# Performance work log

Hardware: AMD Instinct MI355X
Metric: run time of the kernel (lower is better)

Reference implementation:

```python
import jax, jax.numpy as jnp
import numpy as np

N_CLASS, N_SUPPORT, N_QUERY = 64, 5, 64
D_IN, C, WIN = 1024, 128, 5
D = C * WIN * WIN  # 3200, fine-encoder output dim


def setup_inputs() -> dict:
    key = jax.random.key(0)
    ks = jax.random.split(key, 6)
    s = 0.02  # weight init scale
    return {
        "xs": jax.random.normal(ks[0], (N_CLASS, N_SUPPORT, D_IN), jnp.float32),
        "xq": jax.random.normal(ks[1], (N_CLASS, N_QUERY, D_IN), jnp.float32),
        "W_share": jax.random.normal(ks[2], (D_IN, D), jnp.float32) * s,
        "b_share": jnp.zeros((D,), jnp.float32),
        "W_att": jax.random.normal(ks[3], (C, C), jnp.float32) * s,
        "b_att": jnp.zeros((C,), jnp.float32),
        "W_fine": jax.random.normal(ks[4], (D, D), jnp.float32) * s,
        "b_fine": jnp.zeros((D,), jnp.float32),
    }


def reference(xs, xq, W_share, b_share, W_att, b_att, W_fine, b_fine):
    n_class, n_support = xs.shape[0], xs.shape[1]
    n_query = xq.shape[1]
    ns = n_class * n_support

    # concat support + query, run shared encoder
    x = jnp.concatenate([xs.reshape(ns, -1), xq.reshape(n_class * n_query, -1)], axis=0)
    z_share = jax.nn.relu(x @ W_share + b_share)            # [N, D]
    z4 = z_share.reshape(-1, C, WIN, WIN)

    # attention head: spatial mean -> linear -> per-channel logits
    z_att = z4.mean(axis=(2, 3)) @ W_att + b_att            # [N, C]

    diag_c = jax.nn.softmax(z_att[:ns].mean(axis=0)) * C    # [C]
    w = jnp.repeat(diag_c, WIN * WIN)                       # [D] diagonal of learned metric

    # fine encoder (flatten + linear)
    z = z_share @ W_fine + b_fine                           # [N, D]
    z_proto = z[:ns].reshape(n_class, n_support, -1).mean(axis=1)  # [n_class, D]
    zq = z[ns:]                                             # [n, D]

    # attentionMetric with diagonal metric == weighted squared distance:
    # dists[i,j] = sum_d w_d (zq_i - proto_j)^2, expanded to avoid the n*m*d diff tensor
    q2 = (zq * zq) @ w                                      # [n]
    p2 = (z_proto * z_proto) @ w                            # [m]
    cross = (zq * w) @ z_proto.T                            # [n, m]
    dists = q2[:, None] + p2[None, :] - 2.0 * cross         # [n, m]

    log_p_y = jax.nn.log_softmax(-dists, axis=1).reshape(n_class, n_query, n_class)
    target = jnp.arange(n_class)
    tgt = jnp.broadcast_to(target[:, None, None], (n_class, n_query, 1))
    loss_val = -jnp.take_along_axis(log_p_y, tgt, axis=2).mean()
    y_hat = jnp.argmax(log_p_y, axis=2)
    acc_val = (y_hat == target[:, None]).astype(jnp.float32).mean()
    return loss_val, acc_val
```

## Files before the change

### kernel.cpp

```cpp
#include <hip/hip_runtime.h>
#include <math.h>

#define N_CLASS 64
#define N_SUPPORT 5
#define N_QUERY 64
#define D_IN 1024
#define C_CH 128
#define WIN 5
#define D_FEAT 3200
#define NS 320
#define NQ 4096
#define M_ROWS 4416
#define M_PAD 4480

#define ZP_SLICE  (N_CLASS * D_FEAT)
#define GT_SLICE  (128 * D_FEAT)
#define CR_SLICE  (NQ * 128)
#define NKS       10
#define LOSS_BLKS (NQ / 4)

#define PREP_X   4480
#define PREP_WS  800
#define CONV64   2500
#define GEMM8_BLKS (35 * 25)

#define WS_SCALE    64.0f
#define WS_INVSCALE 0.015625f

#define WS_XF8      0u
#define WS_WSF8     4718592u
#define WS_ZSB      8126464u
#define WS_WFB      36388864u
#define WS_WFTB     56868864u
#define WS_ARENA    77348864u
#define WS_UB       98320384u
#define WS_YB       99139584u
#define WS_GT       99958784u
#define WS_WV       100777984u
#define WS_P2       100790784u
#define WS_CVEC     100791296u
#define WS_LPART    100791808u
#define WS_UPOOL    100800128u


typedef __bf16 bf16x8 __attribute__((ext_vector_type(8)));
typedef __bf16 bf16x4 __attribute__((ext_vector_type(4)));
typedef float floatx4 __attribute__((ext_vector_type(4)));
typedef __attribute__((address_space(1))) const void* gptr_t;
typedef __attribute__((address_space(3))) void* lptr_t;

__device__ __forceinline__ float waveReduceSum(float v) {
    for (int off = 32; off > 0; off >>= 1) v += __shfl_xor(v, off, 64);
    return v;
}

__global__ __launch_bounds__(256) void prep_kernel(const float* __restrict__ xs,
                                                   const float* __restrict__ xq,
                                                   const float* __restrict__ W_share,
                                                   unsigned char* __restrict__ Xf8,
                                                   unsigned char* __restrict__ Wsf8)
{
    __shared__ float tile[64][65];
    const int b = blockIdx.x;
    const int t = threadIdx.x;

    if (b < PREP_X) {
        const int e = (b * 256 + t) * 4;
        const int row = e >> 10;
        const int col = e & 1023;
        float4 v = make_float4(0.f, 0.f, 0.f, 0.f);
        if (row < NS)          v = *(const float4*)(xs + (size_t)row * D_IN + col);
        else if (row < M_ROWS) v = *(const float4*)(xq + (size_t)(row - NS) * D_IN + col);
        int p = __builtin_amdgcn_cvt_pk_fp8_f32(v.x, v.y, 0, false);
        p     = __builtin_amdgcn_cvt_pk_fp8_f32(v.z, v.w, p, true);
        const int ocol = col ^ (((row >> 1) & 1) << 3);
        *(int*)(Xf8 + (size_t)row * D_IN + ocol) = p;
        return;
    }
    const int tx = t & 63;
    const int ty = t >> 6;
    const int tb = b - PREP_X;
    const int n0 = (tb % 50) * 64;
    const int k0 = (tb / 50) * 64;
#pragma unroll
    for (int i = ty; i < 64; i += 4)
        tile[i][tx] = W_share[(size_t)(k0 + i) * D_FEAT + n0 + tx];
    __syncthreads();
#pragma unroll
    for (int i = ty; i < 64; i += 4) {
        const int p = __builtin_amdgcn_cvt_pk_fp8_f32(tile[tx][i] * WS_SCALE, 0.f,
                                                      0, false);
        const int n = n0 + i;
        const int k = (k0 + tx) ^ (((n >> 1) & 1) << 3);
        Wsf8[(size_t)n * D_IN + k] = (unsigned char)(p & 0xff);
    }
}

__global__ __launch_bounds__(256, 3) void gemm_fp8_128(const unsigned char* __restrict__ A,
                                                       const unsigned char* __restrict__ Bt,
                                                       const float* __restrict__ bias,
                                                       __bf16* __restrict__ out_bf)
{
    __shared__ __align__(16) unsigned char smem[49152];

    const int t    = threadIdx.x;
    const int lane = t & 63;
    const int w    = t >> 6;
    const int wm   = w >> 1;
    const int wn   = w & 1;

    const int bx = blockIdx.x % 25;
    const int by = blockIdx.x / 25;
    const int bm = by * 128;
    const int bn = bx * 128;

    const int q    = lane >> 4;
    const int r16  = lane & 15;
    const int m3   = (r16 >> 1) & 7;
    const int off0 = (q ^ m3) * 8;

    const int rowA = (wm * 64 + r16) * 64;
    const int rowB = (wn * 64 + r16) * 64;

    const int srow  = t >> 2;
    const int sunit = 16 * ((t & 3) ^ ((srow >> 2) & 3));

    const unsigned char* gA = A  + (size_t)(bm + srow) * D_IN + sunit;
    const unsigned char* gB = Bt + (size_t)(bn + srow) * D_IN + sunit;

    auto stage = [&](int uu, int slot) {
        const unsigned char* ga = gA + uu * 64;
        const unsigned char* gb = gB + uu * 64;
        unsigned char* l = smem + slot * 16384 + t * 16;
        __builtin_amdgcn_global_load_lds((gptr_t)ga,           (lptr_t)l,            16, 0, 0);
        __builtin_amdgcn_global_load_lds((gptr_t)(ga + 65536), (lptr_t)(l + 4096),   16, 0, 0);
        __builtin_amdgcn_global_load_lds((gptr_t)gb,           (lptr_t)(l + 8192),   16, 0, 0);
        __builtin_amdgcn_global_load_lds((gptr_t)(gb + 65536), (lptr_t)(l + 12288),  16, 0, 0);
    };

    floatx4 acc[4][4] = {};
    long av0[4], bv0[4], av1[4], bv1[4];

    auto ld16 = [&](const unsigned char* sa) {
#pragma unroll
        for (int mi = 0; mi < 4; ++mi)
            av0[mi] = *(const long*)(sa + rowA + mi * 1024 + off0);
#pragma unroll
        for (int ni = 0; ni < 4; ++ni)
            bv0[ni] = *(const long*)(sa + 8192 + rowB + ni * 1024 + off0);
#pragma unroll
        for (int mi = 0; mi < 4; ++mi)
            av1[mi] = *(const long*)(sa + rowA + mi * 1024 + (off0 ^ 32));
#pragma unroll
        for (int ni = 0; ni < 4; ++ni)
            bv1[ni] = *(const long*)(sa + 8192 + rowB + ni * 1024 + (off0 ^ 32));
    };
    auto mfma32 = [&]() {
        __builtin_amdgcn_s_setprio(1);
#pragma unroll
        for (int mi = 0; mi < 4; ++mi)
#pragma unroll
            for (int ni = 0; ni < 4; ++ni)
                acc[mi][ni] = __builtin_amdgcn_mfma_f32_16x16x32_fp8_fp8(
                    av0[mi], bv0[ni], acc[mi][ni], 0, 0, 0);
#pragma unroll
        for (int mi = 0; mi < 4; ++mi)
#pragma unroll
            for (int ni = 0; ni < 4; ++ni)
                acc[mi][ni] = __builtin_amdgcn_mfma_f32_16x16x32_fp8_fp8(
                    av1[mi], bv1[ni], acc[mi][ni], 0, 0, 0);
        __builtin_amdgcn_s_setprio(0);
    };

    stage(0, 0);
    stage(1, 1);

    for (int u = 0; u < 14; ++u) {
        const unsigned char* sa = smem + (u % 3) * 16384;
        asm volatile("s_waitcnt vmcnt(4)" ::: "memory");
        __builtin_amdgcn_s_barrier();
        ld16(sa);
        stage(u + 2, (u + 2) % 3);
        asm volatile("s_waitcnt lgkmcnt(0)" ::: "memory");
        mfma32();
    }
    {
        const unsigned char* sa = smem + (14 % 3) * 16384;
        asm volatile("s_waitcnt vmcnt(4)" ::: "memory");
        __builtin_amdgcn_s_barrier();
        ld16(sa);
        asm volatile("s_waitcnt lgkmcnt(0)" ::: "memory");
        mfma32();
    }
    {
        const unsigned char* sa = smem + (15 % 3) * 16384;
        asm volatile("s_waitcnt vmcnt(0)" ::: "memory");
        __builtin_amdgcn_s_barrier();
        ld16(sa);
        asm volatile("s_waitcnt lgkmcnt(0)" ::: "memory");
        mfma32();
    }

    __syncthreads();
    float bcol[4];
#pragma unroll
    for (int ni = 0; ni < 4; ++ni) bcol[ni] = bias[bn + wn * 64 + ni * 16 + r16];
    const int ebase = (wm * 64 + q * 4) * 256 + wn * 128 + r16 * 2;
#pragma unroll
    for (int mi = 0; mi < 4; ++mi)
#pragma unroll
        for (int ni = 0; ni < 4; ++ni) {
            const int cb2 = (ni ^ q) << 5;
#pragma unroll
            for (int reg = 0; reg < 4; ++reg) {
                float v = acc[mi][ni][reg] * WS_INVSCALE + bcol[ni];
                v = fmaxf(v, 0.f);
                *(__bf16*)(smem + ebase + mi * 4096 + reg * 256 + cb2) = (__bf16)v;
            }
        }
    __syncthreads();
#pragma unroll
    for (int ps = 0; ps < 8; ++ps) {
        const int idx  = ps * 256 + t;
        const int row  = idx >> 4;
        const int grow = bm + row;
        if (grow < M_ROWS) {
            const int lb = row * 256 + (((idx & 15) << 4) ^ (((row >> 2) & 3) << 5));
            const int4 d = *(const int4*)(smem + lb);
            *(int4*)((char*)out_bf + ((size_t)grow * D_FEAT + bn + (idx & 15) * 8) * 2) = d;
        }
    }
}

__global__ __launch_bounds__(256) void gemm_bf16(const __bf16* __restrict__ A,
                                                 const __bf16* __restrict__ Bt,
                                                 const float* __restrict__ bias,
                                                 __bf16* __restrict__ out_bf,
                                                 float* __restrict__ out_f32,
                                                 int N, int strideK, int kIters,
                                                 int Mout, int relu, int sliceStride,
                                                 int nbx, int nby, int colLimit,
                                                 const float* __restrict__ attUpool,
                                                 const float* __restrict__ W_att,
                                                 const float* __restrict__ b_att,
                                                 float* __restrict__ wvec)
{
    __shared__ __align__(16) char smem[49152];
    const int t = threadIdx.x;

    if (attUpool != nullptr && blockIdx.x == gridDim.x - 1) {
        float* sW   = (float*)smem;
        float* s_pm = (float*)(smem + 16384);
        float* s_at = (float*)(smem + 16384 + 512);
        float* s_dg = (float*)(smem + 16384 + 1024);
        if (t < C_CH) {
            float a = 0.f;
            for (int p = 0; p < N_CLASS; ++p) a += attUpool[(size_t)p * C_CH + t];
            s_pm[t] = a * (1.0f / (N_CLASS * 25));
        }
        __syncthreads();
        float acc = (t < C_CH) ? b_att[t] : 0.f;
#pragma unroll
        for (int qtr = 0; qtr < 4; ++qtr) {
            const float4* src = (const float4*)(W_att + qtr * 32 * C_CH);
            float4* dst = (float4*)sW;
#pragma unroll
            for (int i = 0; i < 4; ++i) dst[i * 256 + t] = src[i * 256 + t];
            __syncthreads();
            if (t < C_CH) {
#pragma unroll
                for (int k = 0; k < 32; ++k)
                    acc += s_pm[qtr * 32 + k] * sW[k * C_CH + t];
            }
            __syncthreads();
        }
        if (t < C_CH) s_at[t] = acc;
        __syncthreads();
        if (t < C_CH) {
            float m = -INFINITY;
            for (int k = 0; k < C_CH; ++k) m = fmaxf(m, s_at[k]);
            float s = 0.f;
            for (int k = 0; k < C_CH; ++k) s += expf(s_at[k] - m);
            s_dg[t] = expf(acc - m) / s * (float)C_CH;
        }
        __syncthreads();
        for (int j = t; j < D_FEAT; j += 256) wvec[j] = s_dg[j / 25];
        return;
    }

    int bx, by, ks;
    {
        const int nbxy = nbx * nby;
        ks = blockIdx.x / nbxy;
        const int b = blockIdx.x - ks * nbxy;
        const int fg = nbx >> 3;
        const int full = fg * 8 * nby;
        if (b < full) {
            const int g = b / (8 * nby);
            const int r = b - g * 8 * nby;
            bx = g * 8 + (r & 7);
            by = r >> 3;
        } else {
            const int rem = nbx - fg * 8;
            const int r = b - full;
            bx = fg * 8 + r % rem;
            by = r / rem;
        }
    }

    const int lane = t & 63;
    const int w    = t >> 6;
    const int wm   = w >> 1;
    const int wn   = w & 1;
    const int bm   = by * 128;
    const int bn   = bx * 128;

    const int q    = lane >> 4;
    const int r16  = lane & 15;
    const int sw   = (r16 >> 1) & 3;
    const int cA   = (q ^ sw) * 8;

    const int srow   = w * 16 + (lane >> 2);
    const int sglob8 = (((lane & 3) ^ ((lane >> 3) & 3))) * 8;

    const int kBase = ks * kIters * 32;
    floatx4 acc[4][4] = {};

    auto stageb = [&](int ki, int slot) {
        const int k0 = kBase + ki * 32;
        char* base = smem + slot * 16384;
#pragma unroll
        for (int j = 0; j < 2; ++j) {
            const __bf16* ga = A  + (size_t)(bm + j * 64 + srow) * strideK
                                  + k0 + sglob8;
            const __bf16* gb = Bt + (size_t)(bn + j * 64 + srow) * strideK
                                  + k0 + sglob8;
            char* la = base +        j * 4096 + w * 1024;
            char* lb = base + 8192 + j * 4096 + w * 1024;
            __builtin_amdgcn_global_load_lds((gptr_t)ga, (lptr_t)la, 16, 0, 0);
            __builtin_amdgcn_global_load_lds((gptr_t)gb, (lptr_t)lb, 16, 0, 0);
        }
    };

    bf16x8 av[4], bv[4];
    auto ldfrags = [&](const char* base) {
        const __bf16* sAe = (const __bf16*)base;
        const __bf16* sBe = (const __bf16*)(base + 8192);
#pragma unroll
        for (int mi = 0; mi < 4; ++mi)
            av[mi] = *(const bf16x8*)(sAe + ((wm * 64 + mi * 16 + r16) * 32 + cA));
#pragma unroll
        for (int ni = 0; ni < 4; ++ni)
            bv[ni] = *(const bf16x8*)(sBe + ((wn * 64 + ni * 16 + r16) * 32 + cA));
    };
    auto mfma16 = [&]() {
#pragma unroll
        for (int mi = 0; mi < 4; ++mi)
#pragma unroll
            for (int ni = 0; ni < 4; ++ni)
                acc[mi][ni] = __builtin_amdgcn_mfma_f32_16x16x32_bf16(
                    av[mi], bv[ni], acc[mi][ni], 0, 0, 0);
    };

    stageb(0, 0);
    stageb(1, 1);

    for (int u = 0; u < kIters; ++u) {
        const char* base = smem + (u % 3) * 16384;
        if (u + 1 < kIters)
            asm volatile("s_waitcnt vmcnt(4)" ::: "memory");
        else
            asm volatile("s_waitcnt vmcnt(0)" ::: "memory");
        __builtin_amdgcn_s_barrier();
        ldfrags(base);
        if (u + 2 < kIters) stageb(u + 2, (u + 2) % 3);
        asm volatile("s_waitcnt lgkmcnt(0)" ::: "memory");
        mfma16();
    }

#pragma unroll
    for (int ni = 0; ni < 4; ++ni) {
        const int col = bn + wn * 64 + ni * 16 + r16;
        if (col < colLimit) {
            const float bcol = sliceStride ? 0.f : bias[col];
#pragma unroll
            for (int mi = 0; mi < 4; ++mi) {
#pragma unroll
                for (int reg = 0; reg < 4; ++reg) {
                    const int row = bm + wm * 64 + mi * 16 + q * 4 + reg;
                    if (row < Mout) {
                        if (sliceStride) {
                            out_f32[(size_t)ks * sliceStride + (size_t)row * N + col] =
                                acc[mi][ni][reg];
                        } else {
                            float v = acc[mi][ni][reg] + bcol;
                            if (relu) v = fmaxf(v, 0.f);
                            if (out_f32) out_f32[(size_t)row * N + col] = v;
                            else         out_bf [(size_t)row * N + col] = (__bf16)v;
                        }
                    }
                }
            }
        }
    }
}

__global__ __launch_bounds__(256) void ut_conv_kernel(const __bf16* __restrict__ z_share,
                                                      const float* __restrict__ W_fine,
                                                      __bf16* __restrict__ u,
                                                      float* __restrict__ upool,
                                                      __bf16* __restrict__ Wfb,
                                                      __bf16* __restrict__ WfTb)
{
    __shared__ __align__(16) char smem_u[16640];
    const int b = blockIdx.x;
    const int t = threadIdx.x;

    if (b >= 128) {
        float (*tile)[65] = (float(*)[65])smem_u;
        const int tb = b - 128;
        const int tx = t & 63;
        const int ty = t >> 6;
        const int n0 = (tb % 50) * 64;
        const int k0 = (tb / 50) * 64;
#pragma unroll
        for (int i = ty; i < 64; i += 4) {
            const float v = W_fine[(size_t)(k0 + i) * D_FEAT + n0 + tx];
            Wfb[(size_t)(k0 + i) * D_FEAT + n0 + tx] = (__bf16)v;
            tile[i][tx] = v;
        }
        __syncthreads();
#pragma unroll
        for (int i = ty; i < 64; i += 4)
            WfTb[(size_t)(n0 + i) * D_FEAT + k0 + tx] = (__bf16)tile[tx][i];
        return;
    }

    float* srow_ = (float*)smem_u;
    const int p = b;
    if (p >= N_CLASS) {
        for (int k = t; k < D_FEAT; k += 256) u[(size_t)p * D_FEAT + k] = (__bf16)0.f;
        return;
    }
    const __bf16* base = z_share + (size_t)(p * N_SUPPORT) * D_FEAT;
    for (int k = t; k < D_FEAT; k += 256) {
        float s = 0.f;
#pragma unroll
        for (int ss = 0; ss < N_SUPPORT; ++ss) s += (float)base[(size_t)ss * D_FEAT + k];
        s *= (1.0f / N_SUPPORT);
        u[(size_t)p * D_FEAT + k] = (__bf16)s;
        srow_[k] = s;
    }
    __syncthreads();
    if (t < C_CH) {
        float pool = 0.f;
#pragma unroll
        for (int win = 0; win < 25; ++win) pool += srow_[t * 25 + win];
        upool[(size_t)p * C_CH + t] = pool;
    }
}

__global__ __launch_bounds__(256) void y_kernel(const float* __restrict__ zp_part,
                                                const float* __restrict__ wv,
                                                const float* __restrict__ bf,
                                                __bf16* __restrict__ y,
                                                float* __restrict__ p2,
                                                float* __restrict__ cvec)
{
    __shared__ float s_red2[8];
    const int p = blockIdx.x;
    const int t = threadIdx.x;
    if (p >= N_CLASS) {
        for (int j = t; j < D_FEAT; j += 256) y[(size_t)p * D_FEAT + j] = (__bf16)0.f;
        return;
    }
    float s2 = 0.f, sc = 0.f;
    for (int j = t; j < D_FEAT; j += 256) {
        float zpf = bf[j];
#pragma unroll
        for (int ss = 0; ss < NKS; ++ss)
            zpf += zp_part[(size_t)ss * ZP_SLICE + (size_t)p * D_FEAT + j];
        const float wj = wv[j];
        y[(size_t)p * D_FEAT + j] = (__bf16)(wj * zpf);
        s2 += wj * zpf * zpf;
        sc += bf[j] * wj * zpf;
    }
    s2 = waveReduceSum(s2);
    sc = waveReduceSum(sc);
    const int lane = t & 63, wid = t >> 6;
    if (lane == 0) { s_red2[wid] = s2; s_red2[4 + wid] = sc; }
    __syncthreads();
    if (t == 0) {
        p2[p]   = s_red2[0] + s_red2[1] + s_red2[2] + s_red2[3];
        cvec[p] = s_red2[4] + s_red2[5] + s_red2[6] + s_red2[7];
    }
}

__global__ __launch_bounds__(256) void gtsum_kernel(const float* __restrict__ gp,
                                                    __bf16* __restrict__ Gt)
{
    const int i4 = blockIdx.x * 256 + threadIdx.x;
    if (i4 >= GT_SLICE / 4) return;
    float4 s = make_float4(0.f, 0.f, 0.f, 0.f);
#pragma unroll
    for (int ss = 0; ss < NKS; ++ss) {
        const float4 v = *(const float4*)(gp + (size_t)ss * GT_SLICE + i4 * 4);
        s.x += v.x; s.y += v.y; s.z += v.z; s.w += v.w;
    }
    bf16x4 o = { (__bf16)s.x, (__bf16)s.y, (__bf16)s.z, (__bf16)s.w };
    *(bf16x4*)(Gt + (size_t)i4 * 4) = o;
}

__global__ __launch_bounds__(256) void loss_kernel(const float* __restrict__ cross_part,
                                                   const float* __restrict__ p2,
                                                   const float* __restrict__ cvec,
                                                   float* __restrict__ lpart)
{
    __shared__ float s_l[4], s_a[4];
    const int t = threadIdx.x;
    const int lane = t & 63, wid = t >> 6;
    const int i = blockIdx.x * 4 + wid;
    float cr = 0.f;
#pragma unroll
    for (int ss = 0; ss < NKS; ++ss)
        cr += cross_part[(size_t)ss * CR_SLICE + (size_t)i * 128 + lane];
    const float neg = 2.0f * (cr + cvec[lane]) - p2[lane];
    float m = neg;
    for (int off = 32; off > 0; off >>= 1) m = fmaxf(m, __shfl_xor(m, off, 64));
    float e = expf(neg - m);
    float ssum = e;
    for (int off = 32; off > 0; off >>= 1) ssum += __shfl_xor(ssum, off, 64);
    const float lse = m + logf(ssum);
    const int tcls = i >> 6;
    const float negt = __shfl(neg, tcls, 64);
    float v = -neg; int bi = lane;
    for (int off = 32; off > 0; off >>= 1) {
        const float ov = __shfl_xor(v, off, 64);
        const int   oi = __shfl_xor(bi, off, 64);
        if (ov < v || (ov == v && oi < bi)) { v = ov; bi = oi; }
    }
    if (lane == 0) { s_l[wid] = lse - negt; s_a[wid] = (bi == tcls) ? 1.0f : 0.0f; }
    __syncthreads();
    if (t == 0) {
        lpart[blockIdx.x]             = s_l[0] + s_l[1] + s_l[2] + s_l[3];
        lpart[LOSS_BLKS + blockIdx.x] = s_a[0] + s_a[1] + s_a[2] + s_a[3];
    }
}

__global__ __launch_bounds__(256) void writeout_kernel(const float* __restrict__ lpart,
                                                       float* __restrict__ out)
{
    __shared__ float s_red2[8];
    const int t = threadIdx.x;
    float l = 0.f, a = 0.f;
    for (int k = t; k < LOSS_BLKS; k += 256) {
        l += lpart[k];
        a += lpart[LOSS_BLKS + k];
    }
    l = waveReduceSum(l);
    a = waveReduceSum(a);
    const int lane = t & 63, wid = t >> 6;
    if (lane == 0) { s_red2[wid] = l; s_red2[4 + wid] = a; }
    __syncthreads();
    if (t == 0) {
        out[0] = (s_red2[0] + s_red2[1] + s_red2[2] + s_red2[3]) * (1.0f / NQ);
        out[1] = (s_red2[4] + s_red2[5] + s_red2[6] + s_red2[7]) * (1.0f / NQ);
    }
}

extern "C" void kernel_launch(void* const* d_in, const int* in_sizes, int n_in,
                              void* d_out, int out_size, void* d_ws, size_t ws_size,
                              hipStream_t stream)
{
    const float* xs      = (const float*)d_in[0];
    const float* xq      = (const float*)d_in[1];
    const float* W_share = (const float*)d_in[2];
    const float* b_share = (const float*)d_in[3];
    const float* W_att   = (const float*)d_in[4];
    const float* b_att   = (const float*)d_in[5];
    const float* W_fine  = (const float*)d_in[6];
    const float* b_fine  = (const float*)d_in[7];
    float* out = (float*)d_out;

    char* ws = (char*)d_ws;
    unsigned char* Xf8  = (unsigned char*)(ws + WS_XF8);
    unsigned char* Wsf8 = (unsigned char*)(ws + WS_WSF8);
    __bf16* Zsb     = (__bf16*)(ws + WS_ZSB);
    __bf16* Wfb     = (__bf16*)(ws + WS_WFB);
    __bf16* WfTb    = (__bf16*)(ws + WS_WFTB);
    float*  arena   = (float*) (ws + WS_ARENA);
    float*  zp_part = arena;
    float*  gt_part = arena;
    float*  cr_part = arena;
    __bf16* ub      = (__bf16*)(ws + WS_UB);
    __bf16* yb      = (__bf16*)(ws + WS_YB);
    __bf16* Gt      = (__bf16*)(ws + WS_GT);
    float*  wv      = (float*) (ws + WS_WV);
    float*  p2v     = (float*) (ws + WS_P2);
    float*  cvec    = (float*) (ws + WS_CVEC);
    float*  lpart   = (float*) (ws + WS_LPART);
    float*  upool   = (float*) (ws + WS_UPOOL);

    prep_kernel<<<PREP_X + PREP_WS, 256, 0, stream>>>(xs, xq, W_share, Xf8, Wsf8);

    gemm_fp8_128<<<GEMM8_BLKS, 256, 0, stream>>>(Xf8, Wsf8, b_share, Zsb);

    ut_conv_kernel<<<128 + CONV64, 256, 0, stream>>>(Zsb, W_fine, ub, upool,
                                                     Wfb, WfTb);

    gemm_bf16<<<25 * NKS + 1, 256, 0, stream>>>(
        ub, WfTb, nullptr, nullptr, zp_part,
        D_FEAT, D_FEAT, 10, N_CLASS, 0, ZP_SLICE, 25, 1, D_FEAT,
        upool, W_att, b_att, wv);

    y_kernel<<<128, 256, 0, stream>>>(zp_part, wv, b_fine, yb, p2v, cvec);

    gemm_bf16<<<25 * NKS, 256, 0, stream>>>(
        yb, Wfb, nullptr, nullptr, gt_part,
        D_FEAT, D_FEAT, 10, 128, 0, GT_SLICE, 25, 1, D_FEAT,
        nullptr, nullptr, nullptr, nullptr);

    gtsum_kernel<<<(GT_SLICE / 4 + 255) / 256, 256, 0, stream>>>(gt_part, Gt);

    gemm_bf16<<<32 * NKS, 256, 0, stream>>>(
        Zsb + (size_t)NS * D_FEAT, Gt, nullptr, nullptr, cr_part,
        128, D_FEAT, 10, NQ, 0, CR_SLICE, 1, 32, 64,
        nullptr, nullptr, nullptr, nullptr);

    loss_kernel<<<LOSS_BLKS, 256, 0, stream>>>(cr_part, p2v, cvec, lpart);

    writeout_kernel<<<1, 256, 0, stream>>>(lpart, out);
}
```

Baseline: 217.5 us.

## Template bf16 GEMM tile shape to skip padded rows and columns

```diff
diff --git a/kernel.cpp b/kernel.cpp
--- a/kernel.cpp
+++ b/kernel.cpp
@@ -14,7 +14,7 @@
 #define M_PAD 4480
 
 #define ZP_SLICE  (N_CLASS * D_FEAT)
-#define GT_SLICE  (128 * D_FEAT)
+#define GT_SLICE  (N_CLASS * D_FEAT)
 #define CR_SLICE  (NQ * 128)
 #define NKS       10
 #define LOSS_BLKS (NQ / 4)
@@ -232,20 +232,23 @@
     }
 }
 
-__global__ __launch_bounds__(256) void gemm_bf16(const __bf16* __restrict__ A,
-                                                 const __bf16* __restrict__ Bt,
-                                                 const float* __restrict__ bias,
-                                                 __bf16* __restrict__ out_bf,
-                                                 float* __restrict__ out_f32,
-                                                 int N, int strideK, int kIters,
-                                                 int Mout, int relu, int sliceStride,
-                                                 int nbx, int nby, int colLimit,
-                                                 const float* __restrict__ attUpool,
-                                                 const float* __restrict__ W_att,
-                                                 const float* __restrict__ b_att,
-                                                 float* __restrict__ wvec)
-{
-    __shared__ __align__(16) char smem[49152];
+template<int MI, int NI>
+__global__ __launch_bounds__(256) void gemm_bf16_t(const __bf16* __restrict__ A,
+                                                   const __bf16* __restrict__ Bt,
+                                                   float* __restrict__ out_f32,
+                                                   int N, int strideK, int kIters,
+                                                   int Mout, int sliceStride,
+                                                   int nbx, int nby,
+                                                   const float* __restrict__ attUpool,
+                                                   const float* __restrict__ W_att,
+                                                   const float* __restrict__ b_att,
+                                                   float* __restrict__ wvec)
+{
+    constexpr int RA   = (MI == 4) ? 64 : 128;
+    constexpr int RB   = (NI == 4) ? 64 : 128;
+    constexpr int SLOT = (RA + RB) * 64;
+
+    __shared__ __align__(16) char smem[3 * SLOT];
     const int t = threadIdx.x;
 
     if (attUpool != nullptr && blockIdx.x == gridDim.x - 1) {
@@ -293,71 +296,59 @@
         const int nbxy = nbx * nby;
         ks = blockIdx.x / nbxy;
         const int b = blockIdx.x - ks * nbxy;
-        const int fg = nbx >> 3;
-        const int full = fg * 8 * nby;
-        if (b < full) {
-            const int g = b / (8 * nby);
-            const int r = b - g * 8 * nby;
-            bx = g * 8 + (r & 7);
-            by = r >> 3;
-        } else {
-            const int rem = nbx - fg * 8;
-            const int r = b - full;
-            bx = fg * 8 + r % rem;
-            by = r / rem;
-        }
+        bx = b % nbx;
+        by = b / nbx;
     }
 
     const int lane = t & 63;
     const int w    = t >> 6;
-    const int wm   = w >> 1;
-    const int wn   = w & 1;
-    const int bm   = by * 128;
-    const int bn   = bx * 128;
+    const int bm   = by * RA;
+    const int bn   = bx * RB;
 
     const int q    = lane >> 4;
     const int r16  = lane & 15;
     const int sw   = (r16 >> 1) & 3;
     const int cA   = (q ^ sw) * 8;
 
-    const int srow   = w * 16 + (lane >> 2);
-    const int sglob8 = (((lane & 3) ^ ((lane >> 3) & 3))) * 8;
+    const int sglob8 = (((t & 3) ^ ((t >> 3) & 3))) * 8;
 
     const int kBase = ks * kIters * 32;
-    floatx4 acc[4][4] = {};
+    floatx4 acc[MI][NI] = {};
 
     auto stageb = [&](int ki, int slot) {
         const int k0 = kBase + ki * 32;
-        char* base = smem + slot * 16384;
-#pragma unroll
-        for (int j = 0; j < 2; ++j) {
-            const __bf16* ga = A  + (size_t)(bm + j * 64 + srow) * strideK
-                                  + k0 + sglob8;
-            const __bf16* gb = Bt + (size_t)(bn + j * 64 + srow) * strideK
-                                  + k0 + sglob8;
-            char* la = base +        j * 4096 + w * 1024;
-            char* lb = base + 8192 + j * 4096 + w * 1024;
-            __builtin_amdgcn_global_load_lds((gptr_t)ga, (lptr_t)la, 16, 0, 0);
-            __builtin_amdgcn_global_load_lds((gptr_t)gb, (lptr_t)lb, 16, 0, 0);
+        char* base = smem + slot * SLOT;
+#pragma unroll
+        for (int g = 0; g < 3; ++g) {
+            const int rr = g * 64 + (t >> 2);
+            const __bf16* gp;
+            if (g * 64 < RA)
+                gp = A + (size_t)(bm + rr) * strideK + k0 + sglob8;
+            else
+                gp = Bt + (size_t)(bn + (rr - RA)) * strideK + k0 + sglob8;
+            char* l = base + g * 4096 + t * 16;
+            __builtin_amdgcn_global_load_lds((gptr_t)gp, (lptr_t)l, 16, 0, 0);
         }
     };
 
-    bf16x8 av[4], bv[4];
+    bf16x8 av[MI], bv[NI];
     auto ldfrags = [&](const char* base) {
-        const __bf16* sAe = (const __bf16*)base;
-        const __bf16* sBe = (const __bf16*)(base + 8192);
-#pragma unroll
-        for (int mi = 0; mi < 4; ++mi)
-            av[mi] = *(const bf16x8*)(sAe + ((wm * 64 + mi * 16 + r16) * 32 + cA));
-#pragma unroll
-        for (int ni = 0; ni < 4; ++ni)
-            bv[ni] = *(const bf16x8*)(sBe + ((wn * 64 + ni * 16 + r16) * 32 + cA));
+        const __bf16* sA = (const __bf16*)base;
+        const __bf16* sB = (const __bf16*)(base + RA * 64);
+        const int arb = (MI == 2) ? w * 32 : 0;
+        const int brb = (NI == 2) ? w * 32 : 0;
+#pragma unroll
+        for (int mi = 0; mi < MI; ++mi)
+            av[mi] = *(const bf16x8*)(sA + ((arb + mi * 16 + r16) * 32 + cA));
+#pragma unroll
+        for (int ni = 0; ni < NI; ++ni)
+            bv[ni] = *(const bf16x8*)(sB + ((brb + ni * 16 + r16) * 32 + cA));
     };
-    auto mfma16 = [&]() {
-#pragma unroll
-        for (int mi = 0; mi < 4; ++mi)
-#pragma unroll
-            for (int ni = 0; ni < 4; ++ni)
+    auto mfmaT = [&]() {
+#pragma unroll
+        for (int mi = 0; mi < MI; ++mi)
+#pragma unroll
+            for (int ni = 0; ni < NI; ++ni)
                 acc[mi][ni] = __builtin_amdgcn_mfma_f32_16x16x32_bf16(
                     av[mi], bv[ni], acc[mi][ni], 0, 0, 0);
     };
@@ -366,40 +357,31 @@
     stageb(1, 1);
 
     for (int u = 0; u < kIters; ++u) {
-        const char* base = smem + (u % 3) * 16384;
+        const char* base = smem + (u % 3) * SLOT;
         if (u + 1 < kIters)
-            asm volatile("s_waitcnt vmcnt(4)" ::: "memory");
+            asm volatile("s_waitcnt vmcnt(3)" ::: "memory");
         else
             asm volatile("s_waitcnt vmcnt(0)" ::: "memory");
         __builtin_amdgcn_s_barrier();
         ldfrags(base);
         if (u + 2 < kIters) stageb(u + 2, (u + 2) % 3);
         asm volatile("s_waitcnt lgkmcnt(0)" ::: "memory");
-        mfma16();
-    }
-
-#pragma unroll
-    for (int ni = 0; ni < 4; ++ni) {
-        const int col = bn + wn * 64 + ni * 16 + r16;
-        if (col < colLimit) {
-            const float bcol = sliceStride ? 0.f : bias[col];
-#pragma unroll
-            for (int mi = 0; mi < 4; ++mi) {
-#pragma unroll
-                for (int reg = 0; reg < 4; ++reg) {
-                    const int row = bm + wm * 64 + mi * 16 + q * 4 + reg;
-                    if (row < Mout) {
-                        if (sliceStride) {
-                            out_f32[(size_t)ks * sliceStride + (size_t)row * N + col] =
-                                acc[mi][ni][reg];
-                        } else {
-                            float v = acc[mi][ni][reg] + bcol;
-                            if (relu) v = fmaxf(v, 0.f);
-                            if (out_f32) out_f32[(size_t)row * N + col] = v;
-                            else         out_bf [(size_t)row * N + col] = (__bf16)v;
-                        }
-                    }
-                }
+        mfmaT();
+    }
+
+    const int rb0 = bm + ((MI == 2) ? w * 32 : 0);
+    const int cb0 = bn + ((NI == 2) ? w * 32 : 0);
+#pragma unroll
+    for (int ni = 0; ni < NI; ++ni) {
+        const int col = cb0 + ni * 16 + r16;
+#pragma unroll
+        for (int mi = 0; mi < MI; ++mi) {
+#pragma unroll
+            for (int reg = 0; reg < 4; ++reg) {
+                const int row = rb0 + mi * 16 + q * 4 + reg;
+                if (row < Mout)
+                    out_f32[(size_t)ks * sliceStride + (size_t)row * N + col] =
+                        acc[mi][ni][reg];
             }
         }
     }
@@ -416,9 +398,9 @@
     const int b = blockIdx.x;
     const int t = threadIdx.x;
 
-    if (b >= 128) {
+    if (b >= 64) {
         float (*tile)[65] = (float(*)[65])smem_u;
-        const int tb = b - 128;
+        const int tb = b - 64;
         const int tx = t & 63;
         const int ty = t >> 6;
         const int n0 = (tb % 50) * 64;
@@ -438,10 +420,6 @@
 
     float* srow_ = (float*)smem_u;
     const int p = b;
-    if (p >= N_CLASS) {
-        for (int k = t; k < D_FEAT; k += 256) u[(size_t)p * D_FEAT + k] = (__bf16)0.f;
-        return;
-    }
     const __bf16* base = z_share + (size_t)(p * N_SUPPORT) * D_FEAT;
     for (int k = t; k < D_FEAT; k += 256) {
         float s = 0.f;
@@ -470,10 +448,6 @@
     __shared__ float s_red2[8];
     const int p = blockIdx.x;
     const int t = threadIdx.x;
-    if (p >= N_CLASS) {
-        for (int j = t; j < D_FEAT; j += 256) y[(size_t)p * D_FEAT + j] = (__bf16)0.f;
-        return;
-    }
     float s2 = 0.f, sc = 0.f;
     for (int j = t; j < D_FEAT; j += 256) {
         float zpf = bf[j];
@@ -605,26 +579,26 @@
 
     gemm_fp8_128<<<GEMM8_BLKS, 256, 0, stream>>>(Xf8, Wsf8, b_share, Zsb);
 
-    ut_conv_kernel<<<128 + CONV64, 256, 0, stream>>>(Zsb, W_fine, ub, upool,
-                                                     Wfb, WfTb);
-
-    gemm_bf16<<<25 * NKS + 1, 256, 0, stream>>>(
-        ub, WfTb, nullptr, nullptr, zp_part,
-        D_FEAT, D_FEAT, 10, N_CLASS, 0, ZP_SLICE, 25, 1, D_FEAT,
+    ut_conv_kernel<<<64 + CONV64, 256, 0, stream>>>(Zsb, W_fine, ub, upool,
+                                                    Wfb, WfTb);
+
+    gemm_bf16_t<4, 2><<<25 * NKS + 1, 256, 0, stream>>>(
+        ub, WfTb, zp_part,
+        D_FEAT, D_FEAT, 10, N_CLASS, ZP_SLICE, 25, 1,
         upool, W_att, b_att, wv);
 
-    y_kernel<<<128, 256, 0, stream>>>(zp_part, wv, b_fine, yb, p2v, cvec);
-
-    gemm_bf16<<<25 * NKS, 256, 0, stream>>>(
-        yb, Wfb, nullptr, nullptr, gt_part,
-        D_FEAT, D_FEAT, 10, 128, 0, GT_SLICE, 25, 1, D_FEAT,
+    y_kernel<<<64, 256, 0, stream>>>(zp_part, wv, b_fine, yb, p2v, cvec);
+
+    gemm_bf16_t<4, 2><<<25 * NKS, 256, 0, stream>>>(
+        yb, Wfb, gt_part,
+        D_FEAT, D_FEAT, 10, N_CLASS, GT_SLICE, 25, 1,
         nullptr, nullptr, nullptr, nullptr);
 
     gtsum_kernel<<<(GT_SLICE / 4 + 255) / 256, 256, 0, stream>>>(gt_part, Gt);
 
-    gemm_bf16<<<32 * NKS, 256, 0, stream>>>(
-        Zsb + (size_t)NS * D_FEAT, Gt, nullptr, nullptr, cr_part,
-        128, D_FEAT, 10, NQ, 0, CR_SLICE, 1, 32, 64,
+    gemm_bf16_t<2, 4><<<32 * NKS, 256, 0, stream>>>(
+        Zsb + (size_t)NS * D_FEAT, Gt, cr_part,
+        128, D_FEAT, 10, NQ, CR_SLICE, 1, 32,
         nullptr, nullptr, nullptr, nullptr);
 
     loss_kernel<<<LOSS_BLKS, 256, 0, stream>>>(cr_part, p2v, cvec, lpart);
```

After: 211.5 us. -2.8%, faster.
